# Performance work log

Hardware: AMD Instinct MI355X
Metric: run time of the kernel (lower is better)

## Reference

```python
import jax, jax.numpy as jnp
import numpy as np

G = 64      # num graphs
N = 1024    # nodes per graph (equal-sized graphs)
D_IN, D_H, D_OUT = 128, 256, 10


def setup_inputs() -> dict:
    key = jax.random.key(0)
    k1, k2, k3, k4, k5 = jax.random.split(key, 5)
    x = jax.random.normal(k1, (G * N, D_IN), dtype=jnp.float32)
    batch = jnp.repeat(jnp.arange(G, dtype=jnp.int64), N)  # sorted graph ids
    lim1 = 1.0 / np.sqrt(D_IN)
    lim2 = 1.0 / np.sqrt(D_H)
    W1 = jax.random.uniform(k2, (D_IN, D_H), minval=-lim1, maxval=lim1, dtype=jnp.float32)
    b1 = jax.random.uniform(k3, (D_H,), minval=-lim1, maxval=lim1, dtype=jnp.float32)
    W2 = jax.random.uniform(k4, (D_H, D_OUT), minval=-lim2, maxval=lim2, dtype=jnp.float32)
    b2 = jax.random.uniform(k5, (D_OUT,), minval=-lim2, maxval=lim2, dtype=jnp.float32)
    return {"x": x, "batch": batch, "W1": W1, "b1": b1, "W2": W2, "b2": b2}


def reference(x, batch, W1, b1, W2, b2):
    # Equal-sized graphs: reshape node dim into [G, N, d] (batch is sorted).
    xg = x.reshape(G, N, D_IN)
    # Cosine-similarity adjacency per graph, zero diagonal (from RAW features).
    xn = xg * jax.lax.rsqrt(jnp.sum(xg * xg, axis=-1, keepdims=True) + 1e-24)
    adj = jnp.einsum('gnd,gmd->gnm', xn, xn)            # [G, N, N]
    adj = adj * (1.0 - jnp.eye(N, dtype=adj.dtype))
    # fc1 + relu on node features, then adjacency propagation.
    h = jax.nn.relu(xg @ W1 + b1)                       # [G, N, D_H]
    h = jnp.einsum('gnm,gmd->gnd', adj, h)              # [G, N, D_H]
    # fc2, global mean pool over nodes, log-softmax over classes.
    out = h @ W2 + b2                                   # [G, N, D_OUT]
    pooled = jnp.mean(out, axis=1)                      # [G, D_OUT]
    return jax.nn.log_softmax(pooled, axis=-1)
```

## Files before the change

kernel.cpp:

```cpp
#include <hip/hip_runtime.h>
#include <hip/hip_bf16.h>

#define G_ 64
#define N_ 1024
#define DIN 128
#define DH 256
#define DOUT 10

typedef float floatx4 __attribute__((ext_vector_type(4)));
typedef short shortx8 __attribute__((ext_vector_type(8)));

__device__ __forceinline__ ushort f2bf(float f) {
  unsigned u = __builtin_bit_cast(unsigned, f);
  unsigned r = (u + 0x7FFFu + ((u >> 16) & 1u)) >> 16;
  return (ushort)r;
}
__device__ __forceinline__ float bflo(unsigned q) {
  return __builtin_bit_cast(float, q << 16);
}
__device__ __forceinline__ float bfhi(unsigned q) {
  return __builtin_bit_cast(float, q & 0xFFFF0000u);
}

__global__ __launch_bounds__(256) void k1_fused(
    const float* __restrict__ x, const float* __restrict__ W1,
    float* __restrict__ norminv, float* __restrict__ u_part,
    ushort* __restrict__ xb, ushort* __restrict__ w1t) {
  if (blockIdx.x >= 1024) {
    const int wb = blockIdx.x - 1024;
    #pragma unroll
    for (int i = 0; i < 2; ++i) {
      const int idx = wb * 512 + i * 256 + threadIdx.x;
      const int k = idx >> 8, d = idx & 255;
      w1t[d * DIN + k] = f2bf(W1[k * DH + d]);
    }
    return;
  }
  const int tid = threadIdx.x;
  const int wave = tid >> 6;
  const int lane = tid & 63;
  const int half = lane >> 5;
  const int l32 = lane & 31;
  __shared__ float red[8][DIN];
  float a0 = 0.f, a1 = 0.f, a2 = 0.f, a3 = 0.f;
  const int mbase = blockIdx.x * 64 + wave * 16;
  #pragma unroll
  for (int i = 0; i < 8; ++i) {
    const int m = mbase + i * 2 + half;
    const float4 v = ((const float4*)(x + (size_t)m * DIN))[l32];
    float ss = v.x * v.x + v.y * v.y + v.z * v.z + v.w * v.w;
    #pragma unroll
    for (int off = 16; off; off >>= 1) ss += __shfl_xor(ss, off, 64);
    const float ninv = rsqrtf(ss + 1e-24f);
    if (l32 == 0) norminv[m] = ninv;
    uint2 pk;
    pk.x = (unsigned)f2bf(v.x) | ((unsigned)f2bf(v.y) << 16);
    pk.y = (unsigned)f2bf(v.z) | ((unsigned)f2bf(v.w) << 16);
    ((uint2*)(xb + (size_t)m * DIN))[l32] = pk;
    a0 = fmaf(v.x, ninv, a0);
    a1 = fmaf(v.y, ninv, a1);
    a2 = fmaf(v.z, ninv, a2);
    a3 = fmaf(v.w, ninv, a3);
  }
  *(float4*)&red[tid >> 5][l32 * 4] = make_float4(a0, a1, a2, a3);
  __syncthreads();
  if (tid < DIN) {
    float t = 0.f;
    #pragma unroll
    for (int r = 0; r < 8; ++r) t += red[r][tid];
    u_part[blockIdx.x * DIN + tid] = t;
  }
}

__global__ __launch_bounds__(256) void k2_mfma(
    const ushort* __restrict__ xb, const ushort* __restrict__ w1t,
    const float* __restrict__ b1, const float* __restrict__ norminv,
    const float* __restrict__ u_part, float* __restrict__ hw_part) {
  const int g = blockIdx.x >> 4;
  const int mb = (blockIdx.x & 15) << 6;
  const int tid = threadIdx.x;
  const int lane = tid & 63;
  const int wave = tid >> 6;
  const int quad = lane >> 4;
  const int l16 = lane & 15;
  __shared__ float u_lds[DIN];
  __shared__ float s_lds[64];

  if (tid < DIN) {
    float t = 0.f;
    const float* up = u_part + (size_t)(g << 4) * DIN + tid;
    #pragma unroll
    for (int r = 0; r < 16; ++r) t += up[r * DIN];
    u_lds[tid] = t;
  }
  __syncthreads();

  {
    const int nd = tid >> 2;
    const int qq = tid & 3;
    const size_t m = (size_t)(g << 10) + mb + nd;
    const uint4* xr = (const uint4*)(xb + m * DIN + qq * 32);
    float p = 0.f;
    #pragma unroll
    for (int j = 0; j < 4; ++j) {
      const uint4 q = xr[j];
      const float* ub = &u_lds[qq * 32 + j * 8];
      p = fmaf(bflo(q.x), ub[0], p); p = fmaf(bfhi(q.x), ub[1], p);
      p = fmaf(bflo(q.y), ub[2], p); p = fmaf(bfhi(q.y), ub[3], p);
      p = fmaf(bflo(q.z), ub[4], p); p = fmaf(bfhi(q.z), ub[5], p);
      p = fmaf(bflo(q.w), ub[6], p); p = fmaf(bfhi(q.w), ub[7], p);
    }
    p += __shfl_xor(p, 1, 64);
    p += __shfl_xor(p, 2, 64);
    if (qq == 0) s_lds[nd] = p * norminv[m] - 1.0f;
  }
  __syncthreads();

  shortx8 bfr[4][4];
  float b1v[4];
  #pragma unroll
  for (int dt = 0; dt < 4; ++dt) {
    const int d = (wave << 6) + (dt << 4) + l16;
    b1v[dt] = b1[d];
    #pragma unroll
    for (int kt = 0; kt < 4; ++kt)
      bfr[dt][kt] = *(const shortx8*)(w1t + (size_t)d * DIN + (kt << 5) + (quad << 3));
  }

  float wsum[4] = {0.f, 0.f, 0.f, 0.f};
  #pragma unroll
  for (int mt = 0; mt < 4; ++mt) {
    const ushort* ar = xb + ((size_t)(g << 10) + mb + (mt << 4) + l16) * DIN;
    shortx8 af[4];
    #pragma unroll
    for (int kt = 0; kt < 4; ++kt)
      af[kt] = *(const shortx8*)(ar + (kt << 5) + (quad << 3));

    floatx4 acc[4] = {{0.f, 0.f, 0.f, 0.f}, {0.f, 0.f, 0.f, 0.f},
                      {0.f, 0.f, 0.f, 0.f}, {0.f, 0.f, 0.f, 0.f}};
    #pragma unroll
    for (int kt = 0; kt < 4; ++kt)
      #pragma unroll
      for (int dt = 0; dt < 4; ++dt)
        acc[dt] = __builtin_amdgcn_mfma_f32_16x16x32_bf16(af[kt], bfr[dt][kt],
                                                          acc[dt], 0, 0, 0);
    #pragma unroll
    for (int dt = 0; dt < 4; ++dt) {
      float bs = 0.f;
      #pragma unroll
      for (int r = 0; r < 4; ++r) {
        const float h = fmaxf(acc[dt][r] + b1v[dt], 0.f);
        bs = fmaf(s_lds[(mt << 4) + (quad << 2) + r], h, bs);
      }
      wsum[dt] += bs;
    }
  }
  #pragma unroll
  for (int dt = 0; dt < 4; ++dt) {
    float w = wsum[dt];
    w += __shfl_xor(w, 16, 64);
    w += __shfl_xor(w, 32, 64);
    if (quad == 0)
      hw_part[(size_t)blockIdx.x * DH + (wave << 6) + (dt << 4) + l16] = w;
  }
}

__global__ __launch_bounds__(256) void k3_head(
    const float* __restrict__ hw_part, const float* __restrict__ W2,
    const float* __restrict__ b2, float* __restrict__ out) {
  const int g = blockIdx.x;
  const int t = threadIdx.x;
  __shared__ float w2l[DH * DOUT];
  __shared__ float hsum[DH];
  __shared__ float partial[40];
  __shared__ float p[DOUT];
  #pragma unroll
  for (int i = 0; i < (DH * DOUT) / 256; ++i)
    w2l[i * 256 + t] = W2[i * 256 + t];
  {
    float hs = 0.f;
    const float* hp = hw_part + (size_t)(g << 4) * DH + t;
    #pragma unroll
    for (int r = 0; r < 16; ++r) hs += hp[r * DH];
    hsum[t] = hs;
  }
  __syncthreads();
  if (t < 40) {
    const int c = t % 10, q = t / 10;
    const float* hg = hsum + q * 64;
    const float* wg = w2l + (q * 64) * DOUT + c;
    float a = 0.f;
    #pragma unroll
    for (int k = 0; k < 64; ++k) a = fmaf(hg[k], wg[k * DOUT], a);
    partial[t] = a;
  }
  __syncthreads();
  if (t < DOUT) {
    p[t] = (partial[t] + partial[t + 10] + partial[t + 20] + partial[t + 30]) *
               (1.0f / N_) + b2[t];
  }
  __syncthreads();
  if (t < DOUT) {
    float mx = p[0];
    #pragma unroll
    for (int c = 1; c < DOUT; ++c) mx = fmaxf(mx, p[c]);
    float se = 0.f;
    #pragma unroll
    for (int c = 0; c < DOUT; ++c) se += expf(p[c] - mx);
    out[g * DOUT + t] = p[t] - (mx + logf(se));
  }
}

extern "C" void kernel_launch(void* const* d_in, const int* in_sizes, int n_in,
                              void* d_out, int out_size, void* d_ws, size_t ws_size,
                              hipStream_t stream) {
  const float* x  = (const float*)d_in[0];
  const float* W1 = (const float*)d_in[2];
  const float* b1 = (const float*)d_in[3];
  const float* W2 = (const float*)d_in[4];
  const float* b2 = (const float*)d_in[5];
  float* out = (float*)d_out;

  float* u_part  = (float*)d_ws;
  float* hw_part = u_part + 1024 * DIN;
  float* norminv = hw_part + 1024 * DH;
  ushort* xb  = (ushort*)(norminv + (size_t)G_ * N_);
  ushort* w1t = xb + (size_t)G_ * N_ * DIN;

  k1_fused<<<1024 + 64, 256, 0, stream>>>(x, W1, norminv, u_part, xb, w1t);
  k2_mfma<<<G_ * 16, 256, 0, stream>>>(xb, w1t, b1, norminv, u_part, hw_part);
  k3_head<<<G_, 256, 0, stream>>>(hw_part, W2, b2, out);
}
```

Before: 112.5 us.

## Fuse head into MFMA kernel via last-block atomic counter and enlarge row tiles

Drops the separate head kernel launch: each graph's blocks bump an atomic counter, and the last block to finish does the pooled fc2 and log-softmax. The counters are zeroed inside k1. k2 now uses 256 blocks that each cover 256 rows instead of 1024 blocks of 64 rows, and the W1 fragment loads move above the first barrier. This saves one launch and cuts partial sums per graph from 16 to 4, but with only 256 blocks the GPU may be underfilled and the per-block serial work grows.

```diff
diff --git a/kernel.cpp b/kernel.cpp
--- a/kernel.cpp
+++ b/kernel.cpp
@@ -25,9 +25,11 @@
 __global__ __launch_bounds__(256) void k1_fused(
     const float* __restrict__ x, const float* __restrict__ W1,
     float* __restrict__ norminv, float* __restrict__ u_part,
-    ushort* __restrict__ xb, ushort* __restrict__ w1t) {
+    ushort* __restrict__ xb, ushort* __restrict__ w1t,
+    unsigned* __restrict__ cnt) {
   if (blockIdx.x >= 1024) {
     const int wb = blockIdx.x - 1024;
+    if (wb == 63 && threadIdx.x < G_) cnt[threadIdx.x] = 0;
     #pragma unroll
     for (int i = 0; i < 2; ++i) {
       const int idx = wb * 512 + i * 256 + threadIdx.x;
@@ -75,16 +77,20 @@
 __global__ __launch_bounds__(256) void k2_mfma(
     const ushort* __restrict__ xb, const ushort* __restrict__ w1t,
     const float* __restrict__ b1, const float* __restrict__ norminv,
-    const float* __restrict__ u_part, float* __restrict__ hw_part) {
-  const int g = blockIdx.x >> 4;
-  const int mb = (blockIdx.x & 15) << 6;
+    const float* __restrict__ u_part, const float* __restrict__ W2,
+    const float* __restrict__ b2, float* __restrict__ hw_part,
+    unsigned* __restrict__ cnt, float* __restrict__ out) {
+  const int gb = blockIdx.x;
+  const int g = gb >> 2;
+  const int mb0 = (gb & 3) << 8;
   const int tid = threadIdx.x;
   const int lane = tid & 63;
   const int wave = tid >> 6;
   const int quad = lane >> 4;
   const int l16 = lane & 15;
   __shared__ float u_lds[DIN];
-  __shared__ float s_lds[64];
+  __shared__ float s_lds[256];
+  __shared__ unsigned last_flag;
 
   if (tid < DIN) {
     float t = 0.f;
@@ -93,12 +99,23 @@
     for (int r = 0; r < 16; ++r) t += up[r * DIN];
     u_lds[tid] = t;
   }
-  __syncthreads();
-
-  {
+  shortx8 bfr[4][4];
+  float b1v[4];
+  #pragma unroll
+  for (int dt = 0; dt < 4; ++dt) {
+    const int d = (wave << 6) + (dt << 4) + l16;
+    b1v[dt] = b1[d];
+    #pragma unroll
+    for (int kt = 0; kt < 4; ++kt)
+      bfr[dt][kt] = *(const shortx8*)(w1t + (size_t)d * DIN + (kt << 5) + (quad << 3));
+  }
+  __syncthreads();
+
+  #pragma unroll
+  for (int st = 0; st < 4; ++st) {
     const int nd = tid >> 2;
     const int qq = tid & 3;
-    const size_t m = (size_t)(g << 10) + mb + nd;
+    const size_t m = (size_t)(g << 10) + mb0 + (st << 6) + nd;
     const uint4* xr = (const uint4*)(xb + m * DIN + qq * 32);
     float p = 0.f;
     #pragma unroll
@@ -112,25 +129,14 @@
     }
     p += __shfl_xor(p, 1, 64);
     p += __shfl_xor(p, 2, 64);
-    if (qq == 0) s_lds[nd] = p * norminv[m] - 1.0f;
-  }
-  __syncthreads();
-
-  shortx8 bfr[4][4];
-  float b1v[4];
-  #pragma unroll
-  for (int dt = 0; dt < 4; ++dt) {
-    const int d = (wave << 6) + (dt << 4) + l16;
-    b1v[dt] = b1[d];
-    #pragma unroll
-    for (int kt = 0; kt < 4; ++kt)
-      bfr[dt][kt] = *(const shortx8*)(w1t + (size_t)d * DIN + (kt << 5) + (quad << 3));
-  }
+    if (qq == 0) s_lds[(st << 6) + nd] = p * norminv[m] - 1.0f;
+  }
+  __syncthreads();
 
   float wsum[4] = {0.f, 0.f, 0.f, 0.f};
   #pragma unroll
-  for (int mt = 0; mt < 4; ++mt) {
-    const ushort* ar = xb + ((size_t)(g << 10) + mb + (mt << 4) + l16) * DIN;
+  for (int mt = 0; mt < 16; ++mt) {
+    const ushort* ar = xb + ((size_t)(g << 10) + mb0 + (mt << 4) + l16) * DIN;
     shortx8 af[4];
     #pragma unroll
     for (int kt = 0; kt < 4; ++kt)
@@ -161,53 +167,53 @@
     w += __shfl_xor(w, 16, 64);
     w += __shfl_xor(w, 32, 64);
     if (quad == 0)
-      hw_part[(size_t)blockIdx.x * DH + (wave << 6) + (dt << 4) + l16] = w;
-  }
-}
-
-__global__ __launch_bounds__(256) void k3_head(
-    const float* __restrict__ hw_part, const float* __restrict__ W2,
-    const float* __restrict__ b2, float* __restrict__ out) {
-  const int g = blockIdx.x;
-  const int t = threadIdx.x;
+      hw_part[(size_t)gb * DH + (wave << 6) + (dt << 4) + l16] = w;
+  }
+
+  __threadfence();
+  if (tid == 0) last_flag = (atomicAdd(&cnt[g], 1u) == 3u) ? 1u : 0u;
+  __syncthreads();
+  if (!last_flag) return;
+  __threadfence();
+
   __shared__ float w2l[DH * DOUT];
   __shared__ float hsum[DH];
   __shared__ float partial[40];
   __shared__ float p[DOUT];
   #pragma unroll
   for (int i = 0; i < (DH * DOUT) / 256; ++i)
-    w2l[i * 256 + t] = W2[i * 256 + t];
+    w2l[i * 256 + tid] = W2[i * 256 + tid];
   {
     float hs = 0.f;
-    const float* hp = hw_part + (size_t)(g << 4) * DH + t;
-    #pragma unroll
-    for (int r = 0; r < 16; ++r) hs += hp[r * DH];
-    hsum[t] = hs;
-  }
-  __syncthreads();
-  if (t < 40) {
-    const int c = t % 10, q = t / 10;
+    const float* hp = hw_part + (size_t)(g << 2) * DH + tid;
+    #pragma unroll
+    for (int r = 0; r < 4; ++r) hs += hp[r * DH];
+    hsum[tid] = hs;
+  }
+  __syncthreads();
+  if (tid < 40) {
+    const int c = tid % 10, q = tid / 10;
     const float* hg = hsum + q * 64;
     const float* wg = w2l + (q * 64) * DOUT + c;
     float a = 0.f;
     #pragma unroll
     for (int k = 0; k < 64; ++k) a = fmaf(hg[k], wg[k * DOUT], a);
-    partial[t] = a;
-  }
-  __syncthreads();
-  if (t < DOUT) {
-    p[t] = (partial[t] + partial[t + 10] + partial[t + 20] + partial[t + 30]) *
-               (1.0f / N_) + b2[t];
-  }
-  __syncthreads();
-  if (t < DOUT) {
+    partial[tid] = a;
+  }
+  __syncthreads();
+  if (tid < DOUT) {
+    p[tid] = (partial[tid] + partial[tid + 10] + partial[tid + 20] +
+              partial[tid + 30]) * (1.0f / N_) + b2[tid];
+  }
+  __syncthreads();
+  if (tid < DOUT) {
     float mx = p[0];
     #pragma unroll
     for (int c = 1; c < DOUT; ++c) mx = fmaxf(mx, p[c]);
     float se = 0.f;
     #pragma unroll
     for (int c = 0; c < DOUT; ++c) se += expf(p[c] - mx);
-    out[g * DOUT + t] = p[t] - (mx + logf(se));
+    out[g * DOUT + tid] = p[tid] - (mx + logf(se));
   }
 }
 
@@ -223,11 +229,12 @@
 
   float* u_part  = (float*)d_ws;
   float* hw_part = u_part + 1024 * DIN;
-  float* norminv = hw_part + 1024 * DH;
+  float* norminv = hw_part + 256 * DH;
   ushort* xb  = (ushort*)(norminv + (size_t)G_ * N_);
   ushort* w1t = xb + (size_t)G_ * N_ * DIN;
-
-  k1_fused<<<1024 + 64, 256, 0, stream>>>(x, W1, norminv, u_part, xb, w1t);
-  k2_mfma<<<G_ * 16, 256, 0, stream>>>(xb, w1t, b1, norminv, u_part, hw_part);
-  k3_head<<<G_, 256, 0, stream>>>(hw_part, W2, b2, out);
-}
+  unsigned* cnt = (unsigned*)(w1t + DH * DIN);
+
+  k1_fused<<<1024 + 64, 256, 0, stream>>>(x, W1, norminv, u_part, xb, w1t, cnt);
+  k2_mfma<<<256, 256, 0, stream>>>(xb, w1t, b1, norminv, u_part, W2, b2,
+                                   hw_part, cnt, out);
+}
```

Result: slower. 126.3 us (+12.3%).
